# Kernel optimization log

Hardware: AMD Instinct MI355X
Metric: run time of the kernel (lower is better)

Reference implementation:

```python
import jax, jax.numpy as jnp
import numpy as np

NODE_SIZE = 40000
REL_SIZE = 2000
TRIPLE_SIZE = 600000
DIM = 128
DEPTH = 2
EPS = 1e-12


def _xavier(key, shape):
    lim = np.sqrt(6.0 / (shape[-2] + shape[-1]))
    return jax.random.uniform(key, shape, minval=-lim, maxval=lim, dtype=jnp.float32)


def _l2norm(x):
    # matches torch F.normalize(p=2, eps=1e-12)
    return x / jnp.maximum(jnp.linalg.norm(x, axis=-1, keepdims=True), EPS)


def _sparse_softmax(row, vals, n_rows):
    # torch.sparse.softmax over nonzeros of each row
    m = jax.ops.segment_max(vals, row, num_segments=n_rows)
    e = jnp.exp(vals - m[row])
    s = jax.ops.segment_sum(e, row, num_segments=n_rows)
    return e / s[row]


def _avg(adj, emb, n_rows):
    # sparse_coo(ones) -> sparse softmax over rows -> sparse mm  (== mean over neighbors)
    row, col = adj[0], adj[1]
    w = _sparse_softmax(row, jnp.zeros(row.shape, emb.dtype), n_rows)  # softmax of equal values
    return jax.ops.segment_sum(w[:, None] * emb[col], row, num_segments=n_rows)


def _nr_encoder(features, rel_emb, adj, r_index, r_val, triple_size, rel_size, node_size,
                attn, gate, proxy, bias):
    # NR_GraphAttention (Dual-AMN style relational reflection attention)
    row, col = adj[0], adj[1]
    # per-triple relation embedding: sparse [T, R] @ rel_emb
    tri_rel = jax.ops.segment_sum(r_val[:, None] * rel_emb[r_index[1]], r_index[0],
                                  num_segments=triple_size)
    tri_rel = _l2norm(tri_rel)  # [T, DIM]
    feats = jnp.tanh(features)
    outs = [feats]
    for l in range(DEPTH):
        neighs = feats[col]                                            # gather [T, DIM]
        neighs = neighs - 2.0 * jnp.sum(neighs * tri_rel, axis=-1, keepdims=True) * tri_rel
        att = _sparse_softmax(row, tri_rel @ attn[l][:, 0], node_size)  # edge attention
        feats = jnp.tanh(jax.ops.segment_sum(neighs * att[:, None], row,
                                             num_segments=node_size))  # scatter-sum
        outs.append(feats)
    out = jnp.concatenate(outs, axis=-1)                               # [N, DIM*(DEPTH+1)]
    # proxy matching + gating
    pa = jax.nn.softmax(_l2norm(out) @ _l2norm(proxy).T, axis=-1)
    pf = out - pa @ proxy
    g = jax.nn.sigmoid(pf @ gate + bias)
    return g * out + (1.0 - g) * pf


def setup_inputs() -> dict:
    ks = jax.random.split(jax.random.key(0), 16)
    ent_adj = jax.random.randint(ks[0], (2, TRIPLE_SIZE), 0, NODE_SIZE, dtype=jnp.int32)
    rel_adj = jnp.stack([jax.random.randint(ks[1], (TRIPLE_SIZE,), 0, NODE_SIZE, dtype=jnp.int32),
                         jax.random.randint(ks[2], (TRIPLE_SIZE,), 0, REL_SIZE, dtype=jnp.int32)])
    adj_list = jax.random.randint(ks[3], (2, TRIPLE_SIZE), 0, NODE_SIZE, dtype=jnp.int32)
    r_index = jnp.stack([jnp.arange(TRIPLE_SIZE, dtype=jnp.int32),
                         jax.random.randint(ks[4], (TRIPLE_SIZE,), 0, REL_SIZE, dtype=jnp.int32)])
    r_val = jax.random.uniform(ks[5], (TRIPLE_SIZE,), dtype=jnp.float32)
    mask = jnp.ones((NODE_SIZE,), dtype=jnp.int32)
    F3 = DIM * (DEPTH + 1)
    return dict(
        ent_adj=ent_adj, rel_adj=rel_adj, node_size=NODE_SIZE, rel_size=REL_SIZE,
        adj_list=adj_list, r_index=r_index, r_val=r_val, triple_size=TRIPLE_SIZE, mask=mask,
        ent_emb=_xavier(ks[6], (NODE_SIZE, DIM)),
        rel_emb=_xavier(ks[7], (REL_SIZE, DIM)),
        e_attn=_xavier(ks[8], (DEPTH, DIM, 1)), e_gate=_xavier(ks[9], (F3, F3)),
        e_proxy=_xavier(ks[10], (64, F3)), e_bias=jnp.zeros((1, F3), jnp.float32),
        r_attn=_xavier(ks[11], (DEPTH, DIM, 1)), r_gate=_xavier(ks[12], (F3, F3)),
        r_proxy=_xavier(ks[13], (64, F3)), r_bias=jnp.zeros((1, F3), jnp.float32),
    )


def reference(ent_adj, rel_adj, node_size, rel_size, adj_list, r_index, r_val, triple_size, mask,
              ent_emb, rel_emb, e_attn, e_gate, e_proxy, e_bias,
              r_attn, r_gate, r_proxy, r_bias):
    ent_feature = _avg(ent_adj, ent_emb, node_size)   # [N, DIM]
    rel_feature = _avg(rel_adj, rel_emb, node_size)   # [N, DIM]
    ent_feat = _nr_encoder(ent_feature, rel_emb, adj_list, r_index, r_val,
                           triple_size, rel_size, node_size, e_attn, e_gate, e_proxy, e_bias)
    rel_feat = _nr_encoder(rel_feature, rel_emb, adj_list, r_index, r_val,
                           triple_size, rel_size, node_size, r_attn, r_gate, r_proxy, r_bias)
    # dropout_rate = 0.0 -> identity
    return jnp.concatenate([ent_feat, rel_feat], axis=-1)  # [N, 768]
```

## Files before the change

### kernel.cpp

```cpp
#include <hip/hip_runtime.h>
#include <cmath>

#define NNODE 40000
#define NREL  2000
#define NTRI  600000
#define DIMK  128
#define F3    384
#define NPROX 64
#define EPSN  1e-12f

typedef unsigned short ushort_t;
typedef __attribute__((ext_vector_type(8))) short bf16x8;
typedef __attribute__((ext_vector_type(4))) float f32x4;

static __device__ __forceinline__ float waveSum(float v) {
#pragma unroll
    for (int m = 32; m >= 1; m >>= 1) v += __shfl_xor(v, m, 64);
    return v;
}

static __device__ __forceinline__ float bf2f(ushort_t h) {
    return __uint_as_float(((unsigned int)h) << 16);
}

static __device__ __forceinline__ void qreduce4(float4& v) {
#pragma unroll
    for (int m = 16; m <= 32; m <<= 1) {
        v.x += __shfl_xor(v.x, m, 64);
        v.y += __shfl_xor(v.y, m, 64);
        v.z += __shfl_xor(v.z, m, 64);
        v.w += __shfl_xor(v.w, m, 64);
    }
}

__global__ void k_count3(const int* __restrict__ rA, const int* __restrict__ rE,
                         const int* __restrict__ rR, int* __restrict__ dA,
                         int* __restrict__ dE, int* __restrict__ dR) {
    int t = blockIdx.x * 256 + threadIdx.x;
    if (t < NTRI) {
        atomicAdd(&dA[rA[t]], 1);
        atomicAdd(&dE[rE[t]], 1);
        atomicAdd(&dR[rR[t]], 1);
    }
}

__global__ void k_scan_fast(const int* __restrict__ dA, int* __restrict__ oA,
                            const int* __restrict__ dE, int* __restrict__ oE,
                            const int* __restrict__ dR, int* __restrict__ oR) {
    const int* deg = blockIdx.x == 0 ? dA : (blockIdx.x == 1 ? dE : dR);
    int* off = blockIdx.x == 0 ? oA : (blockIdx.x == 1 ? oE : oR);
    __shared__ int wsum[16];
    __shared__ int wpre[16];
    int tid = threadIdx.x;
    int lane = tid & 63, wv = tid >> 6;
    const int CH = 40;
    int base = tid * CH;
    int s = 0;
    for (int i = 0; i < CH; i++) {
        int idx = base + i;
        s += (idx < NNODE) ? deg[idx] : 0;
    }
    int incl = s;
#pragma unroll
    for (int m = 1; m < 64; m <<= 1) {
        int v = __shfl_up(incl, m, 64);
        if (lane >= m) incl += v;
    }
    if (lane == 63) wsum[wv] = incl;
    __syncthreads();
    if (tid < 16) {
        int v = wsum[tid];
#pragma unroll
        for (int m = 1; m < 16; m <<= 1) {
            int u = __shfl_up(v, m, 64);
            if (tid >= m) v += u;
        }
        wpre[tid] = v;
    }
    __syncthreads();
    int waveoff = (wv == 0) ? 0 : wpre[wv - 1];
    int run = waveoff + incl - s;
    for (int i = 0; i < CH; i++) {
        int idx = base + i;
        if (idx < NNODE) {
            off[idx] = run;
            run += deg[idx];
        }
    }
    if (tid == 0) off[NNODE] = wpre[15];
}

__global__ void k_place3(const int* __restrict__ rA, const int* __restrict__ cA,
                         const int* __restrict__ rE, const int* __restrict__ cE,
                         const int* __restrict__ rR, const int* __restrict__ cR,
                         const int* __restrict__ ridx, const float* __restrict__ scalev,
                         const int* __restrict__ oA, const int* __restrict__ oE,
                         const int* __restrict__ oR,
                         int* __restrict__ cntA, int* __restrict__ cntE, int* __restrict__ cntR,
                         int* __restrict__ ePack, float* __restrict__ eSc,
                         int* __restrict__ eColE, int* __restrict__ eColR) {
    int t = blockIdx.x * 256 + threadIdx.x;
    if (t < NTRI) {
        int r = rA[t];
        int p = oA[r] + atomicAdd(&cntA[r], 1);
        ePack[p] = cA[t] | (ridx[t] << 16);
        eSc[p] = scalev[t];
        r = rE[t];
        eColE[oE[r] + atomicAdd(&cntE[r], 1)] = cE[t];
        r = rR[t];
        eColR[oR[r] + atomicAdd(&cntR[r], 1)] = cR[t];
    }
}

__global__ void k_relprep(const float* __restrict__ rel_emb,
                          const float* __restrict__ e_attn, const float* __restrict__ r_attn,
                          float* __restrict__ nrm, float2* __restrict__ attL0,
                          float2* __restrict__ attL1) {
    int r = blockIdx.x;
    int lane = threadIdx.x;
    float a = rel_emb[r * DIMK + lane];
    float b = rel_emb[r * DIMK + 64 + lane];
    float nn = waveSum(a * a + b * b);
    float d0 = waveSum(a * e_attn[lane] + b * e_attn[64 + lane]);
    float d1 = waveSum(a * e_attn[DIMK + lane] + b * e_attn[DIMK + 64 + lane]);
    float d2 = waveSum(a * r_attn[lane] + b * r_attn[64 + lane]);
    float d3 = waveSum(a * r_attn[DIMK + lane] + b * r_attn[DIMK + 64 + lane]);
    if (lane == 0) {
        nrm[r] = sqrtf(nn);
        attL0[r] = make_float2(d0, d2);
        attL1[r] = make_float2(d1, d3);
    }
}

__global__ void k_scale(const int* __restrict__ ridx, const float* __restrict__ rval,
                        const float* __restrict__ nrm, float* __restrict__ scalev) {
    int t = blockIdx.x * 256 + threadIdx.x;
    if (t < NTRI) {
        float v = rval[t];
        float nn = fabsf(v) * nrm[ridx[t]];
        scalev[t] = v / fmaxf(nn, EPSN);
    }
}

__global__ void k_proxyprep(const float* __restrict__ proxy, float* __restrict__ pnT) {
    int k = blockIdx.x;
    int lane = threadIdx.x;
    float v[6];
    float ss = 0.f;
#pragma unroll
    for (int j = 0; j < 6; j++) {
        v[j] = proxy[k * F3 + j * 64 + lane];
        ss += v[j] * v[j];
    }
    ss = waveSum(ss);
    float inv = 1.0f / fmaxf(sqrtf(ss), EPSN);
#pragma unroll
    for (int j = 0; j < 6; j++) pnT[(j * 64 + lane) * NPROX + k] = v[j] * inv;
}

__global__ void k_gateprep(const float* __restrict__ g, ushort_t* __restrict__ th,
                           ushort_t* __restrict__ tl) {
    int k = blockIdx.x;
    int c = threadIdx.x;
    float v = g[(size_t)k * F3 + c];
    unsigned int b = __float_as_uint(v);
    th[(size_t)c * F3 + k] = (ushort_t)(b >> 16);
    float lo = v - __uint_as_float(b & 0xffff0000u);
    tl[(size_t)c * F3 + k] = (ushort_t)(__float_as_uint(lo) >> 16);
}

__global__ __launch_bounds__(256) void k_avg2(
    const int* __restrict__ offE, const int* __restrict__ eColE, const float* __restrict__ ent_emb,
    const int* __restrict__ offR, const int* __restrict__ eColR, const float* __restrict__ rel_emb,
    float* __restrict__ out_e, float* __restrict__ out_r) {
    int gw = (blockIdx.x * blockDim.x + threadIdx.x) >> 6;
    int lane = threadIdx.x & 63;
    if (gw >= 2 * NNODE) return;
    bool isR = gw >= NNODE;
    int wid = isR ? gw - NNODE : gw;
    const int* off = isR ? offR : offE;
    const int* ecol = isR ? eColR : eColE;
    const float4* emb4 = (const float4*)(isR ? rel_emb : ent_emb);
    float* outp = isR ? out_r : out_e;
    int q = lane >> 4, ql = lane & 15;
    int e0 = off[wid], e1 = off[wid + 1];
    float4 aA = {0, 0, 0, 0}, aB = {0, 0, 0, 0};
    for (int base = e0; base < e1; base += 64) {
        int n = min(64, e1 - base);
        int mc = (lane < n) ? ecol[base + lane] : -1;
        for (int j = 0; j < n; j += 4) {
            int e = j + q;
            int c = __shfl(mc, e, 64);
            if (e < n) {
                float4 va = emb4[(size_t)c * 32 + ql];
                float4 vb = emb4[(size_t)c * 32 + 16 + ql];
                aA.x += va.x; aA.y += va.y; aA.z += va.z; aA.w += va.w;
                aB.x += vb.x; aB.y += vb.y; aB.z += vb.z; aB.w += vb.w;
            }
        }
    }
    qreduce4(aA);
    qreduce4(aB);
    if (q == 0) {
        float invd = (e1 > e0) ? 1.0f / (float)(e1 - e0) : 0.0f;
        float4* o = (float4*)outp;
        float4 ra = {tanhf(aA.x * invd), tanhf(aA.y * invd), tanhf(aA.z * invd), tanhf(aA.w * invd)};
        float4 rb = {tanhf(aB.x * invd), tanhf(aB.y * invd), tanhf(aB.z * invd), tanhf(aB.w * invd)};
        o[(size_t)wid * 96 + ql] = ra;
        o[(size_t)wid * 96 + 16 + ql] = rb;
    }
}

__global__ __launch_bounds__(256) void k_agg2(
    const int* __restrict__ off, const int* __restrict__ ePack, const float* __restrict__ eSc,
    const float2* __restrict__ attL, const float* __restrict__ rel_emb,
    float* __restrict__ out_e, float* __restrict__ out_r, int lin) {
    int wid = (blockIdx.x * blockDim.x + threadIdx.x) >> 6;
    int lane = threadIdx.x & 63;
    if (wid >= NNODE) return;
    int q = lane >> 4, ql = lane & 15;
    int e0 = off[wid], e1 = off[wid + 1];
    const float4* rel4 = (const float4*)rel_emb;
    const float4* pe4 = (const float4*)out_e;
    const float4* pr4 = (const float4*)out_r;
    int sA = lin * 32 + ql, sB = lin * 32 + 16 + ql;
    float4 aEa = {0, 0, 0, 0}, aEb = {0, 0, 0, 0}, aRa = {0, 0, 0, 0}, aRb = {0, 0, 0, 0};
    float sE = 0.f, sR = 0.f;
    for (int base = e0; base < e1; base += 64) {
        int n = min(64, e1 - base);
        int pk = 0;
        float sc = 0.f, wE = 0.f, wR = 0.f;
        if (lane < n) {
            pk = ePack[base + lane];
            sc = eSc[base + lane];
            float2 a = attL[pk >> 16];
            wE = __expf(sc * a.x);
            wR = __expf(sc * a.y);
        }
        for (int j = 0; j < n; j += 4) {
            int e = j + q;
            int pke = __shfl(pk, e, 64);
            float sce = __shfl(sc, e, 64);
            float wEe = __shfl(wE, e, 64);
            float wRe = __shfl(wR, e, 64);
            int c = pke & 0xFFFF;
            int r = pke >> 16;
            float4 ra = rel4[(size_t)r * 32 + ql];
            float4 rb = rel4[(size_t)r * 32 + 16 + ql];
            float4 fa = pe4[(size_t)c * 96 + sA];
            float4 fb = pe4[(size_t)c * 96 + sB];
            float4 ga = pr4[(size_t)c * 96 + sA];
            float4 gb = pr4[(size_t)c * 96 + sB];
            float tax = sce * ra.x, tay = sce * ra.y, taz = sce * ra.z, taw = sce * ra.w;
            float tbx = sce * rb.x, tby = sce * rb.y, tbz = sce * rb.z, tbw = sce * rb.w;
            float dE = fa.x * tax + fa.y * tay + fa.z * taz + fa.w * taw +
                       fb.x * tbx + fb.y * tby + fb.z * tbz + fb.w * tbw;
            float dR = ga.x * tax + ga.y * tay + ga.z * taz + ga.w * taw +
                       gb.x * tbx + gb.y * tby + gb.z * tbz + gb.w * tbw;
#pragma unroll
            for (int m = 1; m <= 8; m <<= 1) {
                dE += __shfl_xor(dE, m, 64);
                dR += __shfl_xor(dR, m, 64);
            }
            dE *= 2.f;
            dR *= 2.f;
            aEa.x += wEe * (fa.x - dE * tax);
            aEa.y += wEe * (fa.y - dE * tay);
            aEa.z += wEe * (fa.z - dE * taz);
            aEa.w += wEe * (fa.w - dE * taw);
            aEb.x += wEe * (fb.x - dE * tbx);
            aEb.y += wEe * (fb.y - dE * tby);
            aEb.z += wEe * (fb.z - dE * tbz);
            aEb.w += wEe * (fb.w - dE * tbw);
            aRa.x += wRe * (ga.x - dR * tax);
            aRa.y += wRe * (ga.y - dR * tay);
            aRa.z += wRe * (ga.z - dR * taz);
            aRa.w += wRe * (ga.w - dR * taw);
            aRb.x += wRe * (gb.x - dR * tbx);
            aRb.y += wRe * (gb.y - dR * tby);
            aRb.z += wRe * (gb.z - dR * tbz);
            aRb.w += wRe * (gb.w - dR * tbw);
            sE += wEe;
            sR += wRe;
        }
    }
    qreduce4(aEa);
    qreduce4(aEb);
    qreduce4(aRa);
    qreduce4(aRb);
#pragma unroll
    for (int m = 16; m <= 32; m <<= 1) {
        sE += __shfl_xor(sE, m, 64);
        sR += __shfl_xor(sR, m, 64);
    }
    if (q == 0) {
        float iE = (e1 > e0) ? 1.f / sE : 0.f;
        float4* o = (float4*)out_e;
        float4 wa = {tanhf(aEa.x * iE), tanhf(aEa.y * iE), tanhf(aEa.z * iE), tanhf(aEa.w * iE)};
        float4 wb = {tanhf(aEb.x * iE), tanhf(aEb.y * iE), tanhf(aEb.z * iE), tanhf(aEb.w * iE)};
        o[(size_t)wid * 96 + (lin + 1) * 32 + ql] = wa;
        o[(size_t)wid * 96 + (lin + 1) * 32 + 16 + ql] = wb;
    } else if (q == 1) {
        float iR = (e1 > e0) ? 1.f / sR : 0.f;
        float4* o = (float4*)out_r;
        float4 wa = {tanhf(aRa.x * iR), tanhf(aRa.y * iR), tanhf(aRa.z * iR), tanhf(aRa.w * iR)};
        float4 wb = {tanhf(aRb.x * iR), tanhf(aRb.y * iR), tanhf(aRb.z * iR), tanhf(aRb.w * iR)};
        o[(size_t)wid * 96 + (lin + 1) * 32 + ql] = wa;
        o[(size_t)wid * 96 + (lin + 1) * 32 + 16 + ql] = wb;
    }
}

__global__ void k_scores(const float* __restrict__ outb, const float* __restrict__ pnT,
                         float* __restrict__ pa) {
    __shared__ __align__(16) float As[16][68];
    __shared__ __align__(16) float Bs[16][68];
    __shared__ float Ss[64][65];
    __shared__ float rnS[64];
    int tid = threadIdx.x;
    int row0 = blockIdx.x * 64;
    int kk = tid & 15, rr = tid >> 4;
    int cb = tid & 63, kb = tid >> 6;
    int tx = tid & 15, ty = tid >> 4;
    int c0 = tx * 4, r0 = ty * 4;
    float acc[4][4] = {};
    float ssp[4] = {};
    for (int k0 = 0; k0 < F3; k0 += 16) {
#pragma unroll
        for (int u = 0; u < 4; u++) {
            int r = rr + u * 16;
            float v = outb[(size_t)(row0 + r) * F3 + k0 + kk];
            As[kk][r] = v;
            ssp[u] += v * v;
        }
#pragma unroll
        for (int u = 0; u < 4; u++) {
            int k = kb + u * 4;
            Bs[k][cb] = pnT[(size_t)(k0 + k) * NPROX + cb];
        }
        __syncthreads();
#pragma unroll
        for (int k = 0; k < 16; k++) {
            float4 av = *(const float4*)&As[k][r0];
            float4 bv = *(const float4*)&Bs[k][c0];
            float a[4] = {av.x, av.y, av.z, av.w};
            float b[4] = {bv.x, bv.y, bv.z, bv.w};
#pragma unroll
            for (int i = 0; i < 4; i++)
#pragma unroll
                for (int j = 0; j < 4; j++) acc[i][j] += a[i] * b[j];
        }
        __syncthreads();
    }
#pragma unroll
    for (int u = 0; u < 4; u++) {
        float ss = ssp[u];
#pragma unroll
        for (int m = 1; m < 16; m <<= 1) ss += __shfl_xor(ss, m, 64);
        if (kk == 0) rnS[rr + u * 16] = 1.0f / fmaxf(sqrtf(ss), EPSN);
    }
    __syncthreads();
#pragma unroll
    for (int i = 0; i < 4; i++) {
        float rn = rnS[r0 + i];
#pragma unroll
        for (int j = 0; j < 4; j++) Ss[r0 + i][c0 + j] = acc[i][j] * rn;
    }
    __syncthreads();
    if (tid < 64) {
        int r = tid;
        float m = -1e30f;
        for (int c = 0; c < 64; c++) m = fmaxf(m, Ss[r][c]);
        float s = 0.f;
        for (int c = 0; c < 64; c++) s += expf(Ss[r][c] - m);
        float inv = 1.f / s;
        float* po = pa + (size_t)(row0 + r) * NPROX;
        for (int c = 0; c < 64; c++) po[c] = expf(Ss[r][c] - m) * inv;
    }
}

__global__ void k_pf(const float* __restrict__ pa, const float* __restrict__ proxy,
                     const float* __restrict__ outb, ushort_t* __restrict__ pfh,
                     ushort_t* __restrict__ pfl) {
    __shared__ __align__(16) float As[16][68];
    __shared__ __align__(16) float Bs[16][68];
    int tid = threadIdx.x;
    int row0 = blockIdx.x * 64;
    int col0 = blockIdx.y * 64;
    int kk = tid & 15, rr = tid >> 4;
    int cb = tid & 63, kb = tid >> 6;
    int tx = tid & 15, ty = tid >> 4;
    int c0 = tx * 4, r0 = ty * 4;
    float acc[4][4] = {};
    for (int k0 = 0; k0 < NPROX; k0 += 16) {
#pragma unroll
        for (int u = 0; u < 4; u++) {
            int r = rr + u * 16;
            As[kk][r] = pa[(size_t)(row0 + r) * NPROX + k0 + kk];
        }
#pragma unroll
        for (int u = 0; u < 4; u++) {
            int k = kb + u * 4;
            Bs[k][cb] = proxy[(size_t)(k0 + k) * F3 + col0 + cb];
        }
        __syncthreads();
#pragma unroll
        for (int k = 0; k < 16; k++) {
            float4 av = *(const float4*)&As[k][r0];
            float4 bv = *(const float4*)&Bs[k][c0];
            float a[4] = {av.x, av.y, av.z, av.w};
            float b[4] = {bv.x, bv.y, bv.z, bv.w};
#pragma unroll
            for (int i = 0; i < 4; i++)
#pragma unroll
                for (int j = 0; j < 4; j++) acc[i][j] += a[i] * b[j];
        }
        __syncthreads();
    }
#pragma unroll
    for (int i = 0; i < 4; i++)
#pragma unroll
        for (int j = 0; j < 4; j++) {
            size_t idx = (size_t)(row0 + r0 + i) * F3 + col0 + c0 + j;
            float v = outb[idx] - acc[i][j];
            unsigned int b = __float_as_uint(v);
            pfh[idx] = (ushort_t)(b >> 16);
            float lo = v - __uint_as_float(b & 0xffff0000u);
            pfl[idx] = (ushort_t)(__float_as_uint(lo) >> 16);
        }
}

__global__ __launch_bounds__(256) void k_gate_mfma(
    const ushort_t* __restrict__ pfh, const ushort_t* __restrict__ pfl,
    const ushort_t* __restrict__ gTh, const ushort_t* __restrict__ gTl,
    const float* __restrict__ bias, const float* __restrict__ outb,
    float* __restrict__ dout, int outoff) {
    __shared__ __align__(16) ushort_t AsH[128 * 40];
    __shared__ __align__(16) ushort_t AsL[128 * 40];
    int tid = threadIdx.x;
    int w = tid >> 6, lane = tid & 63;
    int quad = lane >> 4, l16 = lane & 15;
    int wrow = (w >> 1) * 64, wcol = (w & 1) * 64;
    int gr0 = blockIdx.x * 128;
    int cb0 = blockIdx.y * 128;
    f32x4 acc[4][4];
#pragma unroll
    for (int rt = 0; rt < 4; rt++)
#pragma unroll
        for (int ct = 0; ct < 4; ct++) acc[rt][ct] = (f32x4){0.f, 0.f, 0.f, 0.f};

    int srow = tid >> 2, sseg = tid & 3;
    for (int k0 = 0; k0 < F3; k0 += 32) {
        __syncthreads();
#pragma unroll
        for (int u = 0; u < 2; u++) {
            int row = srow + u * 64;
            int gr = gr0 + row;
            uint4 vh = {0, 0, 0, 0}, vl = {0, 0, 0, 0};
            if (gr < NNODE) {
                vh = *(const uint4*)&pfh[(size_t)gr * F3 + k0 + sseg * 8];
                vl = *(const uint4*)&pfl[(size_t)gr * F3 + k0 + sseg * 8];
            }
            *(uint4*)&AsH[row * 40 + sseg * 8] = vh;
            *(uint4*)&AsL[row * 40 + sseg * 8] = vl;
        }
        __syncthreads();
        bf16x8 ah[4], al[4], bh[4], bl[4];
#pragma unroll
        for (int rt = 0; rt < 4; rt++) {
            int ar = wrow + rt * 16 + l16;
            ah[rt] = *(const bf16x8*)&AsH[ar * 40 + quad * 8];
            al[rt] = *(const bf16x8*)&AsL[ar * 40 + quad * 8];
        }
#pragma unroll
        for (int ct = 0; ct < 4; ct++) {
            int bc = cb0 + wcol + ct * 16 + l16;
            bh[ct] = *(const bf16x8*)&gTh[(size_t)bc * F3 + k0 + quad * 8];
            bl[ct] = *(const bf16x8*)&gTl[(size_t)bc * F3 + k0 + quad * 8];
        }
#pragma unroll
        for (int rt = 0; rt < 4; rt++)
#pragma unroll
            for (int ct = 0; ct < 4; ct++) {
                acc[rt][ct] = __builtin_amdgcn_mfma_f32_16x16x32_bf16(ah[rt], bh[ct], acc[rt][ct], 0, 0, 0);
                acc[rt][ct] = __builtin_amdgcn_mfma_f32_16x16x32_bf16(ah[rt], bl[ct], acc[rt][ct], 0, 0, 0);
                acc[rt][ct] = __builtin_amdgcn_mfma_f32_16x16x32_bf16(al[rt], bh[ct], acc[rt][ct], 0, 0, 0);
            }
    }
#pragma unroll
    for (int rt = 0; rt < 4; rt++) {
        int rbase = gr0 + wrow + rt * 16 + quad * 4;
#pragma unroll
        for (int reg = 0; reg < 4; reg++) {
            int row = rbase + reg;
            if (row >= NNODE) continue;
#pragma unroll
            for (int ct = 0; ct < 4; ct++) {
                int c = cb0 + wcol + ct * 16 + l16;
                float x = acc[rt][ct][reg] + bias[c];
                float g = 1.f / (1.f + __expf(-x));
                size_t idx = (size_t)row * F3 + c;
                float pf = bf2f(pfh[idx]) + bf2f(pfl[idx]);
                float o = outb[idx];
                dout[(size_t)row * 768 + outoff + c] = g * o + (1.f - g) * pf;
            }
        }
    }
}

extern "C" void kernel_launch(void* const* d_in, const int* in_sizes, int n_in,
                              void* d_out, int out_size, void* d_ws, size_t ws_size,
                              hipStream_t stream) {
    const int* ent_adj = (const int*)d_in[0];
    const int* rel_adj = (const int*)d_in[1];
    const int* adj_list = (const int*)d_in[4];
    const int* r_index = (const int*)d_in[5];
    const float* r_val = (const float*)d_in[6];
    const float* ent_emb = (const float*)d_in[9];
    const float* rel_emb = (const float*)d_in[10];
    const float* e_attn = (const float*)d_in[11];
    const float* e_gate = (const float*)d_in[12];
    const float* e_proxy = (const float*)d_in[13];
    const float* e_bias = (const float*)d_in[14];
    const float* r_attn = (const float*)d_in[15];
    const float* r_gate = (const float*)d_in[16];
    const float* r_proxy = (const float*)d_in[17];
    const float* r_bias = (const float*)d_in[18];
    float* out = (float*)d_out;

    char* ws = (char*)d_ws;
    size_t off = 0;
    auto alloc = [&](size_t bytes) -> void* {
        off = (off + 255) & ~(size_t)255;
        void* p = ws + off;
        off += bytes;
        return p;
    };

    int* degcur = (int*)alloc(6 * NNODE * sizeof(int));
    int* degA = degcur, *curA = degcur + NNODE;
    int* degE = degcur + 2 * NNODE, *curE = degcur + 3 * NNODE;
    int* degR = degcur + 4 * NNODE, *curR = degcur + 5 * NNODE;
    int* offA = (int*)alloc((NNODE + 1) * sizeof(int));
    int* offE = (int*)alloc((NNODE + 1) * sizeof(int));
    int* offR = (int*)alloc((NNODE + 1) * sizeof(int));
    int* ePack = (int*)alloc(NTRI * sizeof(int));
    float* eSc = (float*)alloc(NTRI * sizeof(float));
    int* eColE = (int*)alloc(NTRI * sizeof(int));
    int* eColR = (int*)alloc(NTRI * sizeof(int));
    float* nrm = (float*)alloc(NREL * sizeof(float));
    float2* attL0 = (float2*)alloc(NREL * sizeof(float2));
    float2* attL1 = (float2*)alloc(NREL * sizeof(float2));
    float* scalev = (float*)alloc(NTRI * sizeof(float));
    float* pnT = (float*)alloc((size_t)F3 * NPROX * sizeof(float));
    ushort_t* gTh = (ushort_t*)alloc((size_t)F3 * F3 * sizeof(ushort_t));
    ushort_t* gTl = (ushort_t*)alloc((size_t)F3 * F3 * sizeof(ushort_t));
    float* pa = (float*)alloc((size_t)NNODE * NPROX * sizeof(float));
    ushort_t* pfh = (ushort_t*)alloc((size_t)NNODE * F3 * sizeof(ushort_t));
    ushort_t* pfl = (ushort_t*)alloc((size_t)NNODE * F3 * sizeof(ushort_t));
    float* out_e = (float*)alloc((size_t)NNODE * F3 * sizeof(float));
    float* out_r = (float*)alloc((size_t)NNODE * F3 * sizeof(float));
    (void)ws_size; (void)in_sizes; (void)n_in; (void)out_size;

    hipMemsetAsync(degcur, 0, 6 * NNODE * sizeof(int), stream);

    int gT = (NTRI + 255) / 256;
    k_count3<<<gT, 256, 0, stream>>>(adj_list, ent_adj, rel_adj, degA, degE, degR);
    k_scan_fast<<<3, 1024, 0, stream>>>(degA, offA, degE, offE, degR, offR);
    k_relprep<<<NREL, 64, 0, stream>>>(rel_emb, e_attn, r_attn, nrm, attL0, attL1);
    k_scale<<<gT, 256, 0, stream>>>(r_index + NTRI, r_val, nrm, scalev);
    k_place3<<<gT, 256, 0, stream>>>(adj_list, adj_list + NTRI, ent_adj, ent_adj + NTRI,
                                     rel_adj, rel_adj + NTRI, r_index + NTRI, scalev,
                                     offA, offE, offR, curA, curE, curR,
                                     ePack, eSc, eColE, eColR);

    k_avg2<<<(2 * NNODE) / 4, 256, 0, stream>>>(offE, eColE, ent_emb, offR, eColR, rel_emb,
                                                out_e, out_r);

    int gW = NNODE / 4;
    k_agg2<<<gW, 256, 0, stream>>>(offA, ePack, eSc, attL0, rel_emb, out_e, out_r, 0);
    k_agg2<<<gW, 256, 0, stream>>>(offA, ePack, eSc, attL1, rel_emb, out_e, out_r, 1);

    dim3 g2(NNODE / 64, F3 / 64);
    dim3 g3((NNODE + 127) / 128, F3 / 128);
    k_proxyprep<<<NPROX, 64, 0, stream>>>(e_proxy, pnT);
    k_gateprep<<<F3, F3, 0, stream>>>(e_gate, gTh, gTl);
    k_scores<<<NNODE / 64, 256, 0, stream>>>(out_e, pnT, pa);
    k_pf<<<g2, 256, 0, stream>>>(pa, e_proxy, out_e, pfh, pfl);
    k_gate_mfma<<<g3, 256, 0, stream>>>(pfh, pfl, gTh, gTl, e_bias, out_e, out, 0);
    k_proxyprep<<<NPROX, 64, 0, stream>>>(r_proxy, pnT);
    k_gateprep<<<F3, F3, 0, stream>>>(r_gate, gTh, gTl);
    k_scores<<<NNODE / 64, 256, 0, stream>>>(out_r, pnT, pa);
    k_pf<<<g2, 256, 0, stream>>>(pa, r_proxy, out_r, pfh, pfl);
    k_gate_mfma<<<g3, 256, 0, stream>>>(pfh, pfl, gTh, gTl, r_bias, out_r, out, 384);
}
```

Measured before the change: 1.059 ms.

## Slice edge placement by row range, fuse scale, pack edges, batch encoder tail

Edge placement now runs in 8 row-range slices, so each pass's scattered writes and atomics touch a narrower destination window. The price is that every slice re-reads all triple indices. The per-triple scale kernel is folded into placement, and the packed column/relation index and scale are stored together as int2 so k_agg2 loads them in one access. Proxy/gate prep and the score, pf and gate GEMMs for both encoders now launch once with a z-dimension of 2, using separate buffers. This cuts launch count and raises parallelism, at the cost of extra workspace.

```diff
diff --git a/kernel.cpp b/kernel.cpp
--- a/kernel.cpp
+++ b/kernel.cpp
@@ -8,6 +8,8 @@
 #define F3    384
 #define NPROX 64
 #define EPSN  1e-12f
+#define NSLICE 8
+#define SLICE_ROWS (NNODE / NSLICE)
 
 typedef unsigned short ushort_t;
 typedef __attribute__((ext_vector_type(8))) short bf16x8;
@@ -90,26 +92,33 @@
     if (tid == 0) off[NNODE] = wpre[15];
 }
 
-__global__ void k_place3(const int* __restrict__ rA, const int* __restrict__ cA,
-                         const int* __restrict__ rE, const int* __restrict__ cE,
-                         const int* __restrict__ rR, const int* __restrict__ cR,
-                         const int* __restrict__ ridx, const float* __restrict__ scalev,
-                         const int* __restrict__ oA, const int* __restrict__ oE,
-                         const int* __restrict__ oR,
-                         int* __restrict__ cntA, int* __restrict__ cntE, int* __restrict__ cntR,
-                         int* __restrict__ ePack, float* __restrict__ eSc,
-                         int* __restrict__ eColE, int* __restrict__ eColR) {
-    int t = blockIdx.x * 256 + threadIdx.x;
-    if (t < NTRI) {
-        int r = rA[t];
+__global__ __launch_bounds__(256) void k_place_sliced(
+    const int* __restrict__ rA, const int* __restrict__ cA,
+    const int* __restrict__ rE, const int* __restrict__ cE,
+    const int* __restrict__ rR, const int* __restrict__ cR,
+    const int* __restrict__ ridx, const float* __restrict__ rval,
+    const float* __restrict__ nrm,
+    const int* __restrict__ oA, const int* __restrict__ oE, const int* __restrict__ oR,
+    int* __restrict__ cntA, int* __restrict__ cntE, int* __restrict__ cntR,
+    int2* __restrict__ ePackSc, int* __restrict__ eColE, int* __restrict__ eColR) {
+    int slice = blockIdx.x & (NSLICE - 1);
+    int t = (blockIdx.x >> 3) * 256 + threadIdx.x;
+    if (t >= NTRI) return;
+    int lo = slice * SLICE_ROWS;
+    int r = rA[t];
+    if ((unsigned)(r - lo) < (unsigned)SLICE_ROWS) {
+        int rid = ridx[t];
+        float v = rval[t];
+        float sc = v / fmaxf(fabsf(v) * nrm[rid], EPSN);
         int p = oA[r] + atomicAdd(&cntA[r], 1);
-        ePack[p] = cA[t] | (ridx[t] << 16);
-        eSc[p] = scalev[t];
-        r = rE[t];
+        ePackSc[p] = make_int2(cA[t] | (rid << 16), __float_as_int(sc));
+    }
+    r = rE[t];
+    if ((unsigned)(r - lo) < (unsigned)SLICE_ROWS)
         eColE[oE[r] + atomicAdd(&cntE[r], 1)] = cE[t];
-        r = rR[t];
+    r = rR[t];
+    if ((unsigned)(r - lo) < (unsigned)SLICE_ROWS)
         eColR[oR[r] + atomicAdd(&cntR[r], 1)] = cR[t];
-    }
 }
 
 __global__ void k_relprep(const float* __restrict__ rel_emb,
@@ -132,18 +141,12 @@
     }
 }
 
-__global__ void k_scale(const int* __restrict__ ridx, const float* __restrict__ rval,
-                        const float* __restrict__ nrm, float* __restrict__ scalev) {
-    int t = blockIdx.x * 256 + threadIdx.x;
-    if (t < NTRI) {
-        float v = rval[t];
-        float nn = fabsf(v) * nrm[ridx[t]];
-        scalev[t] = v / fmaxf(nn, EPSN);
-    }
-}
-
-__global__ void k_proxyprep(const float* __restrict__ proxy, float* __restrict__ pnT) {
-    int k = blockIdx.x;
+__global__ void k_proxyprep2(const float* __restrict__ e_proxy, const float* __restrict__ r_proxy,
+                             float* __restrict__ pnT_e, float* __restrict__ pnT_r) {
+    int enc = blockIdx.x >= NPROX;
+    int k = blockIdx.x & (NPROX - 1);
+    const float* proxy = enc ? r_proxy : e_proxy;
+    float* pnT = enc ? pnT_r : pnT_e;
     int lane = threadIdx.x;
     float v[6];
     float ss = 0.f;
@@ -158,9 +161,14 @@
     for (int j = 0; j < 6; j++) pnT[(j * 64 + lane) * NPROX + k] = v[j] * inv;
 }
 
-__global__ void k_gateprep(const float* __restrict__ g, ushort_t* __restrict__ th,
-                           ushort_t* __restrict__ tl) {
-    int k = blockIdx.x;
+__global__ void k_gateprep2(const float* __restrict__ e_gate, const float* __restrict__ r_gate,
+                            ushort_t* __restrict__ the, ushort_t* __restrict__ tle,
+                            ushort_t* __restrict__ thr, ushort_t* __restrict__ tlr) {
+    int enc = blockIdx.x >= F3;
+    int k = enc ? blockIdx.x - F3 : blockIdx.x;
+    const float* g = enc ? r_gate : e_gate;
+    ushort_t* th = enc ? thr : the;
+    ushort_t* tl = enc ? tlr : tle;
     int c = threadIdx.x;
     float v = g[(size_t)k * F3 + c];
     unsigned int b = __float_as_uint(v);
@@ -212,7 +220,7 @@
 }
 
 __global__ __launch_bounds__(256) void k_agg2(
-    const int* __restrict__ off, const int* __restrict__ ePack, const float* __restrict__ eSc,
+    const int* __restrict__ off, const int2* __restrict__ ePackSc,
     const float2* __restrict__ attL, const float* __restrict__ rel_emb,
     float* __restrict__ out_e, float* __restrict__ out_r, int lin) {
     int wid = (blockIdx.x * blockDim.x + threadIdx.x) >> 6;
@@ -231,8 +239,9 @@
         int pk = 0;
         float sc = 0.f, wE = 0.f, wR = 0.f;
         if (lane < n) {
-            pk = ePack[base + lane];
-            sc = eSc[base + lane];
+            int2 ps = ePackSc[base + lane];
+            pk = ps.x;
+            sc = __int_as_float(ps.y);
             float2 a = attL[pk >> 16];
             wE = __expf(sc * a.x);
             wR = __expf(sc * a.y);
@@ -310,8 +319,12 @@
     }
 }
 
-__global__ void k_scores(const float* __restrict__ outb, const float* __restrict__ pnT,
-                         float* __restrict__ pa) {
+__global__ void k_scores(const float* __restrict__ out_e, const float* __restrict__ out_r,
+                         const float* __restrict__ pnT_e, const float* __restrict__ pnT_r,
+                         float* __restrict__ pa_e, float* __restrict__ pa_r) {
+    const float* outb = blockIdx.z ? out_r : out_e;
+    const float* pnT = blockIdx.z ? pnT_r : pnT_e;
+    float* pa = blockIdx.z ? pa_r : pa_e;
     __shared__ __align__(16) float As[16][68];
     __shared__ __align__(16) float Bs[16][68];
     __shared__ float Ss[64][65];
@@ -378,9 +391,16 @@
     }
 }
 
-__global__ void k_pf(const float* __restrict__ pa, const float* __restrict__ proxy,
-                     const float* __restrict__ outb, ushort_t* __restrict__ pfh,
-                     ushort_t* __restrict__ pfl) {
+__global__ void k_pf(const float* __restrict__ pa_e, const float* __restrict__ pa_r,
+                     const float* __restrict__ e_proxy, const float* __restrict__ r_proxy,
+                     const float* __restrict__ out_e, const float* __restrict__ out_r,
+                     ushort_t* __restrict__ pfh_e, ushort_t* __restrict__ pfl_e,
+                     ushort_t* __restrict__ pfh_r, ushort_t* __restrict__ pfl_r) {
+    const float* pa = blockIdx.z ? pa_r : pa_e;
+    const float* proxy = blockIdx.z ? r_proxy : e_proxy;
+    const float* outb = blockIdx.z ? out_r : out_e;
+    ushort_t* pfh = blockIdx.z ? pfh_r : pfh_e;
+    ushort_t* pfl = blockIdx.z ? pfl_r : pfl_e;
     __shared__ __align__(16) float As[16][68];
     __shared__ __align__(16) float Bs[16][68];
     int tid = threadIdx.x;
@@ -430,10 +450,20 @@
 }
 
 __global__ __launch_bounds__(256) void k_gate_mfma(
-    const ushort_t* __restrict__ pfh, const ushort_t* __restrict__ pfl,
-    const ushort_t* __restrict__ gTh, const ushort_t* __restrict__ gTl,
-    const float* __restrict__ bias, const float* __restrict__ outb,
-    float* __restrict__ dout, int outoff) {
+    const ushort_t* __restrict__ pfh_e, const ushort_t* __restrict__ pfl_e,
+    const ushort_t* __restrict__ pfh_r, const ushort_t* __restrict__ pfl_r,
+    const ushort_t* __restrict__ gTh_e, const ushort_t* __restrict__ gTl_e,
+    const ushort_t* __restrict__ gTh_r, const ushort_t* __restrict__ gTl_r,
+    const float* __restrict__ e_bias, const float* __restrict__ r_bias,
+    const float* __restrict__ out_e, const float* __restrict__ out_r,
+    float* __restrict__ dout) {
+    const ushort_t* pfh = blockIdx.z ? pfh_r : pfh_e;
+    const ushort_t* pfl = blockIdx.z ? pfl_r : pfl_e;
+    const ushort_t* gTh = blockIdx.z ? gTh_r : gTh_e;
+    const ushort_t* gTl = blockIdx.z ? gTl_r : gTl_e;
+    const float* bias = blockIdx.z ? r_bias : e_bias;
+    const float* outb = blockIdx.z ? out_r : out_e;
+    int outoff = blockIdx.z ? F3 : 0;
     __shared__ __align__(16) ushort_t AsH[128 * 40];
     __shared__ __align__(16) ushort_t AsL[128 * 40];
     int tid = threadIdx.x;
@@ -543,20 +573,24 @@
     int* offA = (int*)alloc((NNODE + 1) * sizeof(int));
     int* offE = (int*)alloc((NNODE + 1) * sizeof(int));
     int* offR = (int*)alloc((NNODE + 1) * sizeof(int));
-    int* ePack = (int*)alloc(NTRI * sizeof(int));
-    float* eSc = (float*)alloc(NTRI * sizeof(float));
+    int2* ePackSc = (int2*)alloc(NTRI * sizeof(int2));
     int* eColE = (int*)alloc(NTRI * sizeof(int));
     int* eColR = (int*)alloc(NTRI * sizeof(int));
     float* nrm = (float*)alloc(NREL * sizeof(float));
     float2* attL0 = (float2*)alloc(NREL * sizeof(float2));
     float2* attL1 = (float2*)alloc(NREL * sizeof(float2));
-    float* scalev = (float*)alloc(NTRI * sizeof(float));
-    float* pnT = (float*)alloc((size_t)F3 * NPROX * sizeof(float));
-    ushort_t* gTh = (ushort_t*)alloc((size_t)F3 * F3 * sizeof(ushort_t));
-    ushort_t* gTl = (ushort_t*)alloc((size_t)F3 * F3 * sizeof(ushort_t));
-    float* pa = (float*)alloc((size_t)NNODE * NPROX * sizeof(float));
-    ushort_t* pfh = (ushort_t*)alloc((size_t)NNODE * F3 * sizeof(ushort_t));
-    ushort_t* pfl = (ushort_t*)alloc((size_t)NNODE * F3 * sizeof(ushort_t));
+    float* pnT_e = (float*)alloc((size_t)F3 * NPROX * sizeof(float));
+    float* pnT_r = (float*)alloc((size_t)F3 * NPROX * sizeof(float));
+    ushort_t* gTh_e = (ushort_t*)alloc((size_t)F3 * F3 * sizeof(ushort_t));
+    ushort_t* gTl_e = (ushort_t*)alloc((size_t)F3 * F3 * sizeof(ushort_t));
+    ushort_t* gTh_r = (ushort_t*)alloc((size_t)F3 * F3 * sizeof(ushort_t));
+    ushort_t* gTl_r = (ushort_t*)alloc((size_t)F3 * F3 * sizeof(ushort_t));
+    float* pa_e = (float*)alloc((size_t)NNODE * NPROX * sizeof(float));
+    float* pa_r = (float*)alloc((size_t)NNODE * NPROX * sizeof(float));
+    ushort_t* pfh_e = (ushort_t*)alloc((size_t)NNODE * F3 * sizeof(ushort_t));
+    ushort_t* pfl_e = (ushort_t*)alloc((size_t)NNODE * F3 * sizeof(ushort_t));
+    ushort_t* pfh_r = (ushort_t*)alloc((size_t)NNODE * F3 * sizeof(ushort_t));
+    ushort_t* pfl_r = (ushort_t*)alloc((size_t)NNODE * F3 * sizeof(ushort_t));
     float* out_e = (float*)alloc((size_t)NNODE * F3 * sizeof(float));
     float* out_r = (float*)alloc((size_t)NNODE * F3 * sizeof(float));
     (void)ws_size; (void)in_sizes; (void)n_in; (void)out_size;
@@ -567,29 +601,26 @@
     k_count3<<<gT, 256, 0, stream>>>(adj_list, ent_adj, rel_adj, degA, degE, degR);
     k_scan_fast<<<3, 1024, 0, stream>>>(degA, offA, degE, offE, degR, offR);
     k_relprep<<<NREL, 64, 0, stream>>>(rel_emb, e_attn, r_attn, nrm, attL0, attL1);
-    k_scale<<<gT, 256, 0, stream>>>(r_index + NTRI, r_val, nrm, scalev);
-    k_place3<<<gT, 256, 0, stream>>>(adj_list, adj_list + NTRI, ent_adj, ent_adj + NTRI,
-                                     rel_adj, rel_adj + NTRI, r_index + NTRI, scalev,
-                                     offA, offE, offR, curA, curE, curR,
-                                     ePack, eSc, eColE, eColR);
+    k_place_sliced<<<gT * NSLICE, 256, 0, stream>>>(
+        adj_list, adj_list + NTRI, ent_adj, ent_adj + NTRI, rel_adj, rel_adj + NTRI,
+        r_index + NTRI, r_val, nrm, offA, offE, offR, curA, curE, curR,
+        ePackSc, eColE, eColR);
+    k_proxyprep2<<<2 * NPROX, 64, 0, stream>>>(e_proxy, r_proxy, pnT_e, pnT_r);
+    k_gateprep2<<<2 * F3, F3, 0, stream>>>(e_gate, r_gate, gTh_e, gTl_e, gTh_r, gTl_r);
 
     k_avg2<<<(2 * NNODE) / 4, 256, 0, stream>>>(offE, eColE, ent_emb, offR, eColR, rel_emb,
                                                 out_e, out_r);
 
     int gW = NNODE / 4;
-    k_agg2<<<gW, 256, 0, stream>>>(offA, ePack, eSc, attL0, rel_emb, out_e, out_r, 0);
-    k_agg2<<<gW, 256, 0, stream>>>(offA, ePack, eSc, attL1, rel_emb, out_e, out_r, 1);
-
-    dim3 g2(NNODE / 64, F3 / 64);
-    dim3 g3((NNODE + 127) / 128, F3 / 128);
-    k_proxyprep<<<NPROX, 64, 0, stream>>>(e_proxy, pnT);
-    k_gateprep<<<F3, F3, 0, stream>>>(e_gate, gTh, gTl);
-    k_scores<<<NNODE / 64, 256, 0, stream>>>(out_e, pnT, pa);
-    k_pf<<<g2, 256, 0, stream>>>(pa, e_proxy, out_e, pfh, pfl);
-    k_gate_mfma<<<g3, 256, 0, stream>>>(pfh, pfl, gTh, gTl, e_bias, out_e, out, 0);
-    k_proxyprep<<<NPROX, 64, 0, stream>>>(r_proxy, pnT);
-    k_gateprep<<<F3, F3, 0, stream>>>(r_gate, gTh, gTl);
-    k_scores<<<NNODE / 64, 256, 0, stream>>>(out_r, pnT, pa);
-    k_pf<<<g2, 256, 0, stream>>>(pa, r_proxy, out_r, pfh, pfl);
-    k_gate_mfma<<<g3, 256, 0, stream>>>(pfh, pfl, gTh, gTl, r_bias, out_r, out, 384);
-}
+    k_agg2<<<gW, 256, 0, stream>>>(offA, ePackSc, attL0, rel_emb, out_e, out_r, 0);
+    k_agg2<<<gW, 256, 0, stream>>>(offA, ePackSc, attL1, rel_emb, out_e, out_r, 1);
+
+    dim3 gS(NNODE / 64, 1, 2);
+    dim3 gP(NNODE / 64, F3 / 64, 2);
+    dim3 gG((NNODE + 127) / 128, F3 / 128, 2);
+    k_scores<<<gS, 256, 0, stream>>>(out_e, out_r, pnT_e, pnT_r, pa_e, pa_r);
+    k_pf<<<gP, 256, 0, stream>>>(pa_e, pa_r, e_proxy, r_proxy, out_e, out_r,
+                                 pfh_e, pfl_e, pfh_r, pfl_r);
+    k_gate_mfma<<<gG, 256, 0, stream>>>(pfh_e, pfl_e, pfh_r, pfl_r, gTh_e, gTl_e, gTh_r, gTl_r,
+                                        e_bias, r_bias, out_e, out_r, out);
+}
```

New measurement: 990.7 us. -6.4%, faster.
